# Kernel optimization log

Hardware: AMD Instinct MI355X
Metric: run time of the kernel (lower is better)

The kernel has to match this reference:

```python
import jax, jax.numpy as jnp
import numpy as np

B, T, F, U, H = 256, 512, 128, 256, 64


def setup_inputs() -> dict:
    key = jax.random.key(0)
    k0, k1, k2, k3, k4 = jax.random.split(key, 5)
    x = jax.random.normal(k0, (B, T, F), dtype=jnp.float32)
    # Keras RandomUniform default range (-0.05, 0.05) for LSTM kernel/bias
    kernel = jax.random.uniform(k1, (F, 4 * U), minval=-0.05, maxval=0.05, dtype=jnp.float32)
    rec_kernel = jax.random.uniform(k2, (U, 4 * U), minval=-0.05, maxval=0.05, dtype=jnp.float32)
    bias = jax.random.uniform(k3, (4 * U,), minval=-0.05, maxval=0.05, dtype=jnp.float32)
    # Dense head: glorot-ish scale for the big [T*U, H] weight
    w_out = jax.random.normal(k4, (T * U, H), dtype=jnp.float32) * (1.0 / np.sqrt(T * U))
    b_out = jnp.zeros((H,), dtype=jnp.float32)
    return {"x": x, "kernel": kernel, "rec_kernel": rec_kernel, "bias": bias,
            "w_out": w_out, "b_out": b_out}


def _lstm_swish(x, kernel, rec_kernel, bias):
    """Keras LSTM with activation=swish, recurrent_activation=sigmoid.
    Gate order along last axis: i, f, c(g), o. Returns full hidden sequence [B,T,U]."""
    b, t, _ = x.shape
    u = rec_kernel.shape[0]
    # Precompute input projections for all timesteps: [B,T,4U]
    xz = jnp.einsum('btf,fg->btg', x, kernel) + bias

    def step(carry, xz_t):
        h, c = carry
        z = xz_t + h @ rec_kernel  # [B,4U]
        zi, zf, zg, zo = jnp.split(z, 4, axis=-1)
        i = jax.nn.sigmoid(zi)
        f = jax.nn.sigmoid(zf)
        g = jax.nn.swish(zg)
        o = jax.nn.sigmoid(zo)
        c_new = f * c + i * g
        h_new = o * jax.nn.swish(c_new)
        return (h_new, c_new), h_new

    h0 = jnp.zeros((b, u), dtype=x.dtype)
    c0 = jnp.zeros((b, u), dtype=x.dtype)
    (_, _), hs = jax.lax.scan(step, (h0, c0), jnp.swapaxes(xz, 0, 1))  # hs: [T,B,U]
    return jnp.swapaxes(hs, 0, 1)  # [B,T,U]


def reference(x, kernel, rec_kernel, bias, w_out, b_out):
    seq = _lstm_swish(x, kernel, rec_kernel, bias)        # [B,T,U]
    flat = seq.reshape(seq.shape[0], -1)                   # [B,T*U]
    return flat @ w_out + b_out                            # [B,horizon]
```

## Files before the change

kernel.cpp:

```cpp
#include <hip/hip_runtime.h>
#include <stdint.h>

#define B_ 256
#define T_ 512
#define F_ 128
#define U_ 256
#define H_ 64
#define G4U 1024

typedef __attribute__((ext_vector_type(8))) short short8;
typedef __attribute__((ext_vector_type(4))) float f32x4;
typedef unsigned long long ull;

#define BARRIER_LDS() asm volatile("s_waitcnt lgkmcnt(0)\ns_barrier" ::: "memory")

__device__ __forceinline__ uint16_t f2bf(float f) {
  uint32_t u = __builtin_bit_cast(uint32_t, f);
  u += 0x7fffu + ((u >> 16) & 1u);
  return (uint16_t)(u >> 16);
}
__device__ __forceinline__ float bf2f(uint32_t v) {
  return __builtin_bit_cast(float, (v & 0xffffu) << 16);
}
__device__ __forceinline__ float frcp(float x) {
  float r;
  asm volatile("v_rcp_f32 %0, %1" : "=v"(r) : "v"(x));
  return r;
}
__device__ __forceinline__ float sigm(float z) {
  return frcp(1.0f + __expf(-z));
}
__device__ __forceinline__ ull ald(const ull* p) {
  return __hip_atomic_load(p, __ATOMIC_RELAXED, __HIP_MEMORY_SCOPE_AGENT);
}

__global__ __launch_bounds__(256, 1) void xz_pre(
    const float* __restrict__ x, const float* __restrict__ kern,
    const float* __restrict__ bias, uint16_t* __restrict__ xz,
    int t0, int L)
{
  const int tid  = threadIdx.x;
  const int lane = tid & 63;
  const int q    = tid >> 6;
  const int il   = lane & 15;
  const int bx   = blockIdx.x;
  const int bg   = bx & 15;
  const int hp   = (bx >> 4) & 1;
  const int tc   = bx >> 5;

  __shared__ __align__(16) uint16_t kern_lds[8192 * 8];
  __shared__ __align__(16) uint16_t x_stage[2][4][64][8];

  for (int s = 0; s < 32; ++s) {
    const int slot = tid + s * 256;
    const int l = slot & 63, kt = (slot >> 6) & 3, ctl = (slot >> 8) & 7, qq = slot >> 11;
    const int col = qq * 256 + (hp * 8 + ctl) * 16 + (l & 15);
    const int kb  = kt * 32 + (l >> 4) * 8;
    short8 v;
    #pragma unroll
    for (int j = 0; j < 8; ++j)
      v[j] = (short)f2bf(kern[(size_t)(kb + j) * G4U + col]);
    *(short8*)&kern_lds[(size_t)slot * 8] = v;
  }
  float bias_r[8];
  #pragma unroll
  for (int ctl = 0; ctl < 8; ++ctl)
    bias_r[ctl] = bias[q * 256 + (hp * 8 + ctl) * 16 + il];

  const int xrow = tid & 15, xfb = (tid >> 4) * 8;
  const int xs_kt = xfb >> 5, xs_l = ((xfb >> 3) & 3) * 16 + xrow;

  float xv[8];
  {
    const float* p = x + ((size_t)(bg * 16 + xrow) * T_ + (t0 + tc * 16)) * F_ + xfb;
    #pragma unroll
    for (int j = 0; j < 8; ++j) xv[j] = p[j];
  }
  __syncthreads();

  for (int tt2 = 0; tt2 < 16; ++tt2) {
    const int t = t0 + tc * 16 + tt2;
    const int bb = tt2 & 1;
    {
      uint16_t* d = &x_stage[bb][xs_kt][xs_l][0];
      #pragma unroll
      for (int j = 0; j < 8; ++j) d[j] = f2bf(xv[j]);
    }
    BARRIER_LDS();
    {
      const int tn = (tt2 < 15) ? t + 1 : t;
      const float* p = x + ((size_t)(bg * 16 + xrow) * T_ + tn) * F_ + xfb;
      #pragma unroll
      for (int j = 0; j < 8; ++j) xv[j] = p[j];
    }
    f32x4 acc[8];
    #pragma unroll
    for (int ctl = 0; ctl < 8; ++ctl)
      acc[ctl] = (f32x4){bias_r[ctl], bias_r[ctl], bias_r[ctl], bias_r[ctl]};
    #pragma unroll
    for (int kt = 0; kt < 4; ++kt) {
      short8 a = *(const short8*)&x_stage[bb][kt][lane][0];
      #pragma unroll
      for (int ctl = 0; ctl < 8; ++ctl) {
        short8 b = *(const short8*)&kern_lds[(size_t)(((q * 8 + ctl) * 4 + kt) * 64 + lane) * 8];
        acc[ctl] = __builtin_amdgcn_mfma_f32_16x16x32_bf16(a, b, acc[ctl], 0, 0, 0);
      }
    }
    uint16_t* ob = xz + (size_t)(bg * L + (t - t0)) * 16384;
    #pragma unroll
    for (int ctl = 0; ctl < 8; ++ctl) {
      const int wd = hp * 8 + ctl;
      const uint32_t lo = (uint32_t)f2bf(acc[ctl][0]) | ((uint32_t)f2bf(acc[ctl][1]) << 16);
      const uint32_t hi = (uint32_t)f2bf(acc[ctl][2]) | ((uint32_t)f2bf(acc[ctl][3]) << 16);
      *(ull*)(ob + (size_t)(wd * 4 + q) * 256 + lane * 4) = (ull)lo | ((ull)hi << 32);
    }
  }
}

__global__ __launch_bounds__(512, 2) void lstm_pair(
    const float* __restrict__ rker, uint16_t* __restrict__ seq,
    ull* __restrict__ hbuf, const uint16_t* __restrict__ xz,
    float* __restrict__ cstbuf, int t0, int L)
{
  const int tid  = threadIdx.x;
  const int lane = tid & 63;
  const int wv   = tid >> 6;
  const int il   = lane & 15;
  const int rg   = lane >> 4;
  const int bg   = blockIdx.x & 15;
  const int m    = blockIdx.x >> 4;

  __shared__ __align__(16) uint16_t h_stage[2][8][64][8];

  short8 wf[4][8];
  #pragma unroll
  for (int q = 0; q < 4; ++q) {
    const int gcol = q * U_ + m * 128 + wv * 16 + il;
    #pragma unroll
    for (int kk = 0; kk < 8; ++kk) {
      const int ktg = ((kk & 4) ? (m ^ 1) : m) * 4 + (kk & 3);
      short8 v;
      #pragma unroll
      for (int j = 0; j < 8; ++j)
        v[j] = (short)f2bf(rker[(size_t)(ktg * 32 + rg * 8 + j) * G4U + gcol]);
      wf[q][kk] = v;
    }
  }

  const int u_loc = wv * 16 + il;
  const int Ua  = m * 128 + u_loc;
  const int kta = Ua >> 5, ga = ((Ua & 31) >> 3) * 16, posa = Ua & 7;

  ull* const pub_s = hbuf + (size_t)(bg * 2 + m) * 2048;
  const ull* const pub_p = hbuf + (size_t)(bg * 2 + (m ^ 1)) * 2048;

  const int up_u = tid >> 2;
  const int up_rb = (tid & 3) * 4;

  float cst[4];
  if (t0 == 0) {
    #pragma unroll
    for (int j = 0; j < 4; ++j) cst[j] = 0.f;
  } else {
    #pragma unroll
    for (int j = 0; j < 4; ++j)
      cst[j] = cstbuf[(size_t)(bg * 16 + rg * 4 + j) * U_ + Ua];
    const ull* op = pub_s + (size_t)((t0 - 1) & 1) * 1024 + tid * 2;
    const ull o0 = ald(op), o1 = ald(op + 1);
    const int U  = m * 128 + up_u;
    const int kt = U >> 5, g = ((U & 31) >> 3) * 16, pos = U & 7;
    h_stage[(t0 - 1) & 1][kt][g + up_rb + 0][pos] = (uint16_t)o0;
    h_stage[(t0 - 1) & 1][kt][g + up_rb + 1][pos] = (uint16_t)(o0 >> 16);
    h_stage[(t0 - 1) & 1][kt][g + up_rb + 2][pos] = (uint16_t)o1;
    h_stage[(t0 - 1) & 1][kt][g + up_rb + 3][pos] = (uint16_t)(o1 >> 16);
  }
  __syncthreads();

  const uint16_t* const pzbase = xz + (size_t)bg * L * 16384
                               + (size_t)((m * 8 + wv) * 4) * 256 + lane * 4;
  ull zc[4];
  #pragma unroll
  for (int q = 0; q < 4; ++q) zc[q] = *(const ull*)(pzbase + q * 256);

  for (int tt = 0; tt < L; ++tt) {
    const int t = t0 + tt;
    const ull* pp = pub_p + (size_t)((t - 1) & 1) * 1024 + tid * 2;
    ull pv0 = 0, pv1 = 0;
    if (t > 0) {
      pv0 = ald(pp); pv1 = ald(pp + 1);
      __builtin_amdgcn_sched_barrier(0);
    }
    f32x4 acc[4];
    #pragma unroll
    for (int q = 0; q < 4; ++q) {
      const uint32_t lo = (uint32_t)zc[q];
      const uint32_t hi = (uint32_t)(zc[q] >> 32);
      acc[q][0] = bf2f(lo); acc[q][1] = bf2f(lo >> 16);
      acc[q][2] = bf2f(hi); acc[q][3] = bf2f(hi >> 16);
    }
    {
      const int ntt = (tt + 1 < L) ? tt + 1 : tt;
      const uint16_t* pn = pzbase + (size_t)ntt * 16384;
      #pragma unroll
      for (int q = 0; q < 4; ++q) zc[q] = *(const ull*)(pn + q * 256);
    }
    if (t > 0) {
      const int p_ = (t - 1) & 1;
      #pragma unroll
      for (int kk = 0; kk < 4; ++kk) {
        short8 a = *(const short8*)&h_stage[p_][m * 4 + kk][lane][0];
        #pragma unroll
        for (int q = 0; q < 4; ++q)
          acc[q] = __builtin_amdgcn_mfma_f32_16x16x32_bf16(a, wf[q][kk], acc[q], 0, 0, 0);
      }
      const uint32_t expt = (uint32_t)t;
      while (((uint32_t)(pv0 >> 32) != expt) | ((uint32_t)(pv1 >> 32) != expt)) {
        pv0 = ald(pp); pv1 = ald(pp + 1);
      }
      const int U  = (m ^ 1) * 128 + up_u;
      const int kt = U >> 5, g = ((U & 31) >> 3) * 16, pos = U & 7;
      h_stage[p_][kt][g + up_rb + 0][pos] = (uint16_t)pv0;
      h_stage[p_][kt][g + up_rb + 1][pos] = (uint16_t)(pv0 >> 16);
      h_stage[p_][kt][g + up_rb + 2][pos] = (uint16_t)pv1;
      h_stage[p_][kt][g + up_rb + 3][pos] = (uint16_t)(pv1 >> 16);
    }
    BARRIER_LDS();
    if (t > 0) {
      const int p_ = (t - 1) & 1;
      #pragma unroll
      for (int kk = 0; kk < 4; ++kk) {
        short8 a = *(const short8*)&h_stage[p_][(m ^ 1) * 4 + kk][lane][0];
        #pragma unroll
        for (int q = 0; q < 4; ++q)
          acc[q] = __builtin_amdgcn_mfma_f32_16x16x32_bf16(a, wf[q][4 + kk], acc[q], 0, 0, 0);
      }
    }
    {
      uint16_t b16[4];
      #pragma unroll
      for (int j = 0; j < 4; ++j) {
        const float zi = acc[0][j], zf = acc[1][j];
        const float zg = acc[2][j], zo = acc[3][j];
        const float ii = sigm(zi), ff = sigm(zf);
        const float gg = zg * sigm(zg), oo = sigm(zo);
        const float c  = ff * cst[j] + ii * gg;
        cst[j] = c;
        b16[j] = f2bf(oo * (c * sigm(c)));
      }
      const int s2 = t & 1;
      ull* pw = pub_s + (size_t)s2 * 1024 + (size_t)u_loc * 8 + rg * 2;
      const ull tg = (ull)(uint32_t)(t + 1) << 32;
      __hip_atomic_store(pw,     (ull)((uint32_t)b16[0] | ((uint32_t)b16[1] << 16)) | tg,
                         __ATOMIC_RELAXED, __HIP_MEMORY_SCOPE_AGENT);
      __hip_atomic_store(pw + 1, (ull)((uint32_t)b16[2] | ((uint32_t)b16[3] << 16)) | tg,
                         __ATOMIC_RELAXED, __HIP_MEMORY_SCOPE_AGENT);
      #pragma unroll
      for (int j = 0; j < 4; ++j) {
        h_stage[s2][kta][ga + rg * 4 + j][posa] = b16[j];
        seq[((size_t)(bg * 16 + rg * 4 + j) * T_ + t) * U_ + Ua] = b16[j];
      }
    }
    BARRIER_LDS();
  }
  #pragma unroll
  for (int j = 0; j < 4; ++j)
    cstbuf[(size_t)(bg * 16 + rg * 4 + j) * U_ + Ua] = cst[j];
}

__global__ __launch_bounds__(512, 2) void lstm_fallback(
    const float* __restrict__ x, const float* __restrict__ kern,
    const float* __restrict__ rker, const float* __restrict__ bias,
    uint16_t* __restrict__ seq, ull* __restrict__ hbuf)
{
  const int tid  = threadIdx.x;
  const int lane = tid & 63;
  const int wv   = tid >> 6;
  const int il   = lane & 15;
  const int rg   = lane >> 4;
  const int bg   = blockIdx.x & 15;
  const int m    = blockIdx.x >> 4;

  __shared__ __align__(16) uint16_t x_stage[4][64][8];
  __shared__ __align__(16) uint16_t h_stage[2][8][64][8];
  __shared__ __align__(16) uint16_t kern_lds[8192 * 8];

  short8 wf[4][8];
  float  bias_r[4];
  #pragma unroll
  for (int q = 0; q < 4; ++q) {
    const int gcol = q * U_ + m * 128 + wv * 16 + il;
    bias_r[q] = bias[gcol];
    #pragma unroll
    for (int kk = 0; kk < 8; ++kk) {
      const int ktg = ((kk & 4) ? (m ^ 1) : m) * 4 + (kk & 3);
      short8 v;
      #pragma unroll
      for (int j = 0; j < 8; ++j)
        v[j] = (short)f2bf(rker[(size_t)(ktg * 32 + rg * 8 + j) * G4U + gcol]);
      wf[q][kk] = v;
    }
  }
  for (int s = 0; s < 16; ++s) {
    const int slot = tid + s * 512;
    const int ln = slot & 63, kt = (slot >> 6) & 3, ct = slot >> 8;
    const int col = (ct >> 3) * U_ + m * 128 + (ct & 7) * 16 + (ln & 15);
    const int kb  = kt * 32 + (ln >> 4) * 8;
    short8 v;
    #pragma unroll
    for (int j = 0; j < 8; ++j)
      v[j] = (short)f2bf(kern[(size_t)(kb + j) * G4U + col]);
    *(short8*)&kern_lds[(size_t)slot * 8] = v;
  }
  const int xkt = tid >> 7;
  const int xln = (tid >> 1) & 63;
  const int xj0 = (tid & 1) * 4;
  const int xrow = xln & 15;
  const int xk0  = xkt * 32 + (xln >> 4) * 8 + xj0;
  const int Ua  = m * 128 + wv * 16 + il;
  const int kta = Ua >> 5, ga = ((Ua & 31) >> 3) * 16, posa = Ua & 7;
  ull* const pub_s = hbuf + (size_t)(bg * 2 + m) * 2048;
  const ull* const pub_p = hbuf + (size_t)(bg * 2 + (m ^ 1)) * 2048;
  float cst[4];
  #pragma unroll
  for (int j = 0; j < 4; ++j) cst[j] = 0.f;
  float xp[4];
  {
    const float* p = x + ((size_t)(bg * 16 + xrow) * T_ + 0) * F_ + xk0;
    #pragma unroll
    for (int j = 0; j < 4; ++j) xp[j] = p[j];
    uint16_t* d = (uint16_t*)x_stage + tid * 4;
    #pragma unroll
    for (int j = 0; j < 4; ++j) d[j] = f2bf(xp[j]);
  }
  __syncthreads();
  for (int t = 0; t < T_; ++t) {
    const ull* pp = pub_p + (size_t)((t - 1) & 1) * 1024 + tid * 2;
    ull pv0 = 0, pv1 = 0;
    if (t > 0) {
      pv0 = ald(pp); pv1 = ald(pp + 1);
      __builtin_amdgcn_sched_barrier(0);
    }
    {
      const int tn = (t + 1 < T_) ? t + 1 : t;
      const float* p = x + ((size_t)(bg * 16 + xrow) * T_ + tn) * F_ + xk0;
      #pragma unroll
      for (int j = 0; j < 4; ++j) xp[j] = p[j];
    }
    f32x4 acc[4];
    #pragma unroll
    for (int q = 0; q < 4; ++q)
      acc[q] = (f32x4){bias_r[q], bias_r[q], bias_r[q], bias_r[q]};
    #pragma unroll
    for (int kt = 0; kt < 4; ++kt) {
      short8 a = *(const short8*)&x_stage[kt][lane][0];
      #pragma unroll
      for (int q = 0; q < 4; ++q) {
        short8 b = *(const short8*)&kern_lds[(size_t)(((q * 8 + wv) * 4 + kt) * 64 + lane) * 8];
        acc[q] = __builtin_amdgcn_mfma_f32_16x16x32_bf16(a, b, acc[q], 0, 0, 0);
      }
    }
    if (t > 0) {
      const int p_ = (t - 1) & 1;
      #pragma unroll
      for (int kk = 0; kk < 4; ++kk) {
        short8 a = *(const short8*)&h_stage[p_][m * 4 + kk][lane][0];
        #pragma unroll
        for (int q = 0; q < 4; ++q)
          acc[q] = __builtin_amdgcn_mfma_f32_16x16x32_bf16(a, wf[q][kk], acc[q], 0, 0, 0);
      }
      const uint32_t expt = (uint32_t)t;
      while (((uint32_t)(pv0 >> 32) != expt) | ((uint32_t)(pv1 >> 32) != expt)) {
        pv0 = ald(pp); pv1 = ald(pp + 1);
      }
      const int u_loc = tid >> 2;
      const int U  = (m ^ 1) * 128 + u_loc;
      const int kt = U >> 5, g = ((U & 31) >> 3) * 16, pos = U & 7;
      const int rb = (tid & 3) * 4;
      h_stage[p_][kt][g + rb + 0][pos] = (uint16_t)pv0;
      h_stage[p_][kt][g + rb + 1][pos] = (uint16_t)(pv0 >> 16);
      h_stage[p_][kt][g + rb + 2][pos] = (uint16_t)pv1;
      h_stage[p_][kt][g + rb + 3][pos] = (uint16_t)(pv1 >> 16);
    }
    BARRIER_LDS();
    if (t > 0) {
      const int p_ = (t - 1) & 1;
      #pragma unroll
      for (int kk = 0; kk < 4; ++kk) {
        short8 a = *(const short8*)&h_stage[p_][(m ^ 1) * 4 + kk][lane][0];
        #pragma unroll
        for (int q = 0; q < 4; ++q)
          acc[q] = __builtin_amdgcn_mfma_f32_16x16x32_bf16(a, wf[q][4 + kk], acc[q], 0, 0, 0);
      }
    }
    {
      uint16_t* d = (uint16_t*)x_stage + tid * 4;
      #pragma unroll
      for (int j = 0; j < 4; ++j) d[j] = f2bf(xp[j]);
    }
    {
      uint16_t b16[4];
      #pragma unroll
      for (int j = 0; j < 4; ++j) {
        const float zi = acc[0][j], zf = acc[1][j];
        const float zg = acc[2][j], zo = acc[3][j];
        const float ii = sigm(zi), ff = sigm(zf);
        const float gg = zg * sigm(zg), oo = sigm(zo);
        const float c  = ff * cst[j] + ii * gg;
        cst[j] = c;
        b16[j] = f2bf(oo * (c * sigm(c)));
      }
      const int s2 = t & 1;
      ull* pw = pub_s + (size_t)s2 * 1024 + (size_t)(wv * 16 + il) * 8 + rg * 2;
      const ull tg = (ull)(uint32_t)(t + 1) << 32;
      __hip_atomic_store(pw,     (ull)((uint32_t)b16[0] | ((uint32_t)b16[1] << 16)) | tg,
                         __ATOMIC_RELAXED, __HIP_MEMORY_SCOPE_AGENT);
      __hip_atomic_store(pw + 1, (ull)((uint32_t)b16[2] | ((uint32_t)b16[3] << 16)) | tg,
                         __ATOMIC_RELAXED, __HIP_MEMORY_SCOPE_AGENT);
      #pragma unroll
      for (int j = 0; j < 4; ++j) {
        h_stage[s2][kta][ga + rg * 4 + j][posa] = b16[j];
        seq[((size_t)(bg * 16 + rg * 4 + j) * T_ + t) * U_ + Ua] = b16[j];
      }
    }
    BARRIER_LDS();
  }
}

__global__ __launch_bounds__(256, 1) void head_kernel(
    const uint16_t* __restrict__ seq, const float* __restrict__ w_out,
    float* __restrict__ partials)
{
  const int g    = blockIdx.x;
  const int tid  = threadIdx.x;
  const int lane = tid & 63;
  const int wv   = tid >> 6;

  f32x4 acc[4][4];
  #pragma unroll
  for (int i = 0; i < 4; ++i)
    #pragma unroll
    for (int c = 0; c < 4; ++c) acc[i][c] = (f32x4){0.f, 0.f, 0.f, 0.f};

  for (int ks = 0; ks < 64; ++ks) {
    const int krow = g * 2048 + ks * 32 + (lane >> 4) * 8;
    short8 bf[4];
    #pragma unroll
    for (int c = 0; c < 4; ++c) {
      short8 v;
      #pragma unroll
      for (int j = 0; j < 8; ++j)
        v[j] = (short)f2bf(w_out[(size_t)(krow + j) * H_ + c * 16 + (lane & 15)]);
      bf[c] = v;
    }
    #pragma unroll
    for (int i = 0; i < 4; ++i) {
      const int b = (wv * 4 + i) * 16 + (lane & 15);
      short8 a = *(const short8*)(seq + (size_t)b * (T_ * U_) + krow);
      #pragma unroll
      for (int c = 0; c < 4; ++c)
        acc[i][c] = __builtin_amdgcn_mfma_f32_16x16x32_bf16(a, bf[c], acc[i][c], 0, 0, 0);
    }
  }
  #pragma unroll
  for (int i = 0; i < 4; ++i)
    #pragma unroll
    for (int c = 0; c < 4; ++c)
      #pragma unroll
      for (int r = 0; r < 4; ++r) {
        const int b = wv * 64 + i * 16 + (lane >> 4) * 4 + r;
        partials[((size_t)g * B_ + b) * H_ + c * 16 + (lane & 15)] = acc[i][c][r];
      }
}

__global__ void reduce_kernel(const float* __restrict__ partials,
                              const float* __restrict__ b_out,
                              float* __restrict__ out)
{
  const int i = blockIdx.x * 256 + threadIdx.x;
  float s = b_out[i & (H_ - 1)];
  #pragma unroll 8
  for (int g = 0; g < 64; ++g) s += partials[(size_t)g * (B_ * H_) + i];
  out[i] = s;
}

extern "C" void kernel_launch(void* const* d_in, const int* in_sizes, int n_in,
                              void* d_out, int out_size, void* d_ws, size_t ws_size,
                              hipStream_t stream) {
  (void)in_sizes; (void)n_in; (void)out_size;
  const float* x     = (const float*)d_in[0];
  const float* kern  = (const float*)d_in[1];
  const float* rker  = (const float*)d_in[2];
  const float* bias  = (const float*)d_in[3];
  const float* w_out = (const float*)d_in[4];
  const float* b_out = (const float*)d_in[5];
  float* out = (float*)d_out;

  char* ws = (char*)d_ws;
  const size_t seq_bytes  = (size_t)B_ * T_ * U_ * 2;
  const size_t hbuf_bytes = (size_t)32 * 2048 * 8;
  const size_t part_bytes = (size_t)64 * B_ * H_ * 4;
  const size_t cst_bytes  = (size_t)B_ * U_ * 4;
  uint16_t* seq      = (uint16_t*)ws;
  ull*      hbuf     = (ull*)(ws + seq_bytes);
  float*    partials = (float*)(ws + seq_bytes + hbuf_bytes);
  float*    cstbuf   = (float*)(ws + seq_bytes + hbuf_bytes + part_bytes);
  const size_t xz_off = seq_bytes + hbuf_bytes + part_bytes + cst_bytes;
  uint16_t* xzbuf = (uint16_t*)(ws + xz_off);

  int L = 0;
  const int cand[4] = {128, 64, 32, 16};
  for (int i = 0; i < 4; ++i) {
    if (ws_size >= xz_off + (size_t)cand[i] * 524288) { L = cand[i]; break; }
  }

  hipMemsetAsync(hbuf, 0, hbuf_bytes, stream);

  if (L > 0) {
    for (int t0 = 0; t0 < T_; t0 += L) {
      xz_pre<<<2 * L, 256, 0, stream>>>(x, kern, bias, xzbuf, t0, L);
      lstm_pair<<<32, 512, 0, stream>>>(rker, seq, hbuf, xzbuf, cstbuf, t0, L);
    }
  } else {
    lstm_fallback<<<32, 512, 0, stream>>>(x, kern, rker, bias, seq, hbuf);
  }
  head_kernel<<<64, 256, 0, stream>>>(seq, w_out, partials);
  reduce_kernel<<<64, 256, 0, stream>>>(partials, b_out, out);
}
```

Measured before the change: 1.193 ms.

## Split batch rows into two interleaved groups to overlap peer exchange with compute

The recurrent kernel's 16 batch rows per block are split into two half-groups (A and B), each with its own LDS staging buffer and its own published hidden-state slots. While waiting for the peer block's half-B values, the block finishes gate math for half A and publishes it, so cross-block communication latency overlaps with useful work. Each half still runs the full MFMA on all 16 rows but keeps only two of them, which doubles MFMA work and adds an extra barrier per step in exchange for a shorter critical path.

```diff
diff --git a/kernel.cpp b/kernel.cpp
--- a/kernel.cpp
+++ b/kernel.cpp
@@ -117,7 +117,7 @@
   }
 }
 
-__global__ __launch_bounds__(512, 2) void lstm_pair(
+__global__ __launch_bounds__(512, 2) void lstm_pair2(
     const float* __restrict__ rker, uint16_t* __restrict__ seq,
     ull* __restrict__ hbuf, const uint16_t* __restrict__ xz,
     float* __restrict__ cstbuf, int t0, int L)
@@ -129,8 +129,11 @@
   const int rg   = lane >> 4;
   const int bg   = blockIdx.x & 15;
   const int m    = blockIdx.x >> 4;
-
-  __shared__ __align__(16) uint16_t h_stage[2][8][64][8];
+  const int bgm  = bg * 2 + m;
+  const int pgm  = bg * 2 + (m ^ 1);
+
+  __shared__ __align__(16) uint16_t hA[2][8][64][8];
+  __shared__ __align__(16) uint16_t hB[2][8][64][8];
 
   short8 wf[4][8];
   #pragma unroll
@@ -151,30 +154,44 @@
   const int Ua  = m * 128 + u_loc;
   const int kta = Ua >> 5, ga = ((Ua & 31) >> 3) * 16, posa = Ua & 7;
 
-  ull* const pub_s = hbuf + (size_t)(bg * 2 + m) * 2048;
-  const ull* const pub_p = hbuf + (size_t)(bg * 2 + (m ^ 1)) * 2048;
-
-  const int up_u = tid >> 2;
-  const int up_rb = (tid & 3) * 4;
-
-  float cst[4];
+  const int cu  = tid >> 2;
+  const int cp  = (tid & 3) * 4;
+  const int Up  = (m ^ 1) * 128 + cu;
+  const int upkt = Up >> 5, upg = ((Up & 31) >> 3) * 16, uppos = Up & 7;
+  const int Uo  = m * 128 + cu;
+  const int uokt = Uo >> 5, uog = ((Uo & 31) >> 3) * 16, uopos = Uo & 7;
+
+  ull* const pubA = hbuf + (size_t)((bgm * 2 + 0) * 2) * 512;
+  ull* const pubB = hbuf + (size_t)((bgm * 2 + 1) * 2) * 512;
+  const ull* const peerA = hbuf + (size_t)((pgm * 2 + 0) * 2) * 512;
+  const ull* const peerB = hbuf + (size_t)((pgm * 2 + 1) * 2) * 512;
+
+  {
+    ull* z0 = (ull*)hA;  ull* z1 = (ull*)hB;
+    #pragma unroll
+    for (int k = 0; k < 4; ++k) { z0[tid + k * 512] = 0; z1[tid + k * 512] = 0; }
+  }
+
+  float cA0, cA1, cB0, cB1;
   if (t0 == 0) {
-    #pragma unroll
-    for (int j = 0; j < 4; ++j) cst[j] = 0.f;
+    cA0 = cA1 = cB0 = cB1 = 0.f;
   } else {
-    #pragma unroll
-    for (int j = 0; j < 4; ++j)
-      cst[j] = cstbuf[(size_t)(bg * 16 + rg * 4 + j) * U_ + Ua];
-    const ull* op = pub_s + (size_t)((t0 - 1) & 1) * 1024 + tid * 2;
-    const ull o0 = ald(op), o1 = ald(op + 1);
-    const int U  = m * 128 + up_u;
-    const int kt = U >> 5, g = ((U & 31) >> 3) * 16, pos = U & 7;
-    h_stage[(t0 - 1) & 1][kt][g + up_rb + 0][pos] = (uint16_t)o0;
-    h_stage[(t0 - 1) & 1][kt][g + up_rb + 1][pos] = (uint16_t)(o0 >> 16);
-    h_stage[(t0 - 1) & 1][kt][g + up_rb + 2][pos] = (uint16_t)o1;
-    h_stage[(t0 - 1) & 1][kt][g + up_rb + 3][pos] = (uint16_t)(o1 >> 16);
+    cA0 = cstbuf[(size_t)(bg * 16 + rg * 4 + 0) * U_ + Ua];
+    cA1 = cstbuf[(size_t)(bg * 16 + rg * 4 + 1) * U_ + Ua];
+    cB0 = cstbuf[(size_t)(bg * 16 + rg * 4 + 2) * U_ + Ua];
+    cB1 = cstbuf[(size_t)(bg * 16 + rg * 4 + 3) * U_ + Ua];
   }
   __syncthreads();
+  if (t0 > 0) {
+    const int rp = (t0 - 1) & 1;
+    const ull oA = ald(pubA + (size_t)rp * 512 + tid);
+    const ull oB = ald(pubB + (size_t)rp * 512 + tid);
+    hA[rp][uokt][uog + cp + 0][uopos] = (uint16_t)oA;
+    hA[rp][uokt][uog + cp + 1][uopos] = (uint16_t)(oA >> 16);
+    hB[rp][uokt][uog + cp + 2][uopos] = (uint16_t)oB;
+    hB[rp][uokt][uog + cp + 3][uopos] = (uint16_t)(oB >> 16);
+    __syncthreads();
+  }
 
   const uint16_t* const pzbase = xz + (size_t)bg * L * 16384
                                + (size_t)((m * 8 + wv) * 4) * 256 + lane * 4;
@@ -183,20 +200,24 @@
   for (int q = 0; q < 4; ++q) zc[q] = *(const ull*)(pzbase + q * 256);
 
   for (int tt = 0; tt < L; ++tt) {
-    const int t = t0 + tt;
-    const ull* pp = pub_p + (size_t)((t - 1) & 1) * 1024 + tid * 2;
-    ull pv0 = 0, pv1 = 0;
-    if (t > 0) {
-      pv0 = ald(pp); pv1 = ald(pp + 1);
+    const int t  = t0 + tt;
+    const int pb = (t - 1) & 1, cb = t & 1;
+    const ull* ppA = peerA + (size_t)pb * 512 + tid;
+    const ull* ppB = peerB + (size_t)pb * 512 + tid;
+    ull pvA = 0, pvB = 0;
+    if (t > 0) {
+      pvA = ald(ppA); pvB = ald(ppB);
       __builtin_amdgcn_sched_barrier(0);
     }
-    f32x4 acc[4];
+    f32x4 accA[4], accB[4];
     #pragma unroll
     for (int q = 0; q < 4; ++q) {
       const uint32_t lo = (uint32_t)zc[q];
       const uint32_t hi = (uint32_t)(zc[q] >> 32);
-      acc[q][0] = bf2f(lo); acc[q][1] = bf2f(lo >> 16);
-      acc[q][2] = bf2f(hi); acc[q][3] = bf2f(hi >> 16);
+      f32x4 z;
+      z[0] = bf2f(lo); z[1] = bf2f(lo >> 16);
+      z[2] = bf2f(hi); z[3] = bf2f(hi >> 16);
+      accA[q] = z; accB[q] = z;
     }
     {
       const int ntt = (tt + 1 < L) ? tt + 1 : tt;
@@ -205,66 +226,93 @@
       for (int q = 0; q < 4; ++q) zc[q] = *(const ull*)(pn + q * 256);
     }
     if (t > 0) {
-      const int p_ = (t - 1) & 1;
       #pragma unroll
       for (int kk = 0; kk < 4; ++kk) {
-        short8 a = *(const short8*)&h_stage[p_][m * 4 + kk][lane][0];
+        short8 aA = *(const short8*)&hA[pb][m * 4 + kk][lane][0];
         #pragma unroll
         for (int q = 0; q < 4; ++q)
-          acc[q] = __builtin_amdgcn_mfma_f32_16x16x32_bf16(a, wf[q][kk], acc[q], 0, 0, 0);
-      }
-      const uint32_t expt = (uint32_t)t;
-      while (((uint32_t)(pv0 >> 32) != expt) | ((uint32_t)(pv1 >> 32) != expt)) {
-        pv0 = ald(pp); pv1 = ald(pp + 1);
-      }
-      const int U  = (m ^ 1) * 128 + up_u;
-      const int kt = U >> 5, g = ((U & 31) >> 3) * 16, pos = U & 7;
-      h_stage[p_][kt][g + up_rb + 0][pos] = (uint16_t)pv0;
-      h_stage[p_][kt][g + up_rb + 1][pos] = (uint16_t)(pv0 >> 16);
-      h_stage[p_][kt][g + up_rb + 2][pos] = (uint16_t)pv1;
-      h_stage[p_][kt][g + up_rb + 3][pos] = (uint16_t)(pv1 >> 16);
-    }
-    BARRIER_LDS();
-    if (t > 0) {
-      const int p_ = (t - 1) & 1;
+          accA[q] = __builtin_amdgcn_mfma_f32_16x16x32_bf16(aA, wf[q][kk], accA[q], 0, 0, 0);
+      }
       #pragma unroll
       for (int kk = 0; kk < 4; ++kk) {
-        short8 a = *(const short8*)&h_stage[p_][(m ^ 1) * 4 + kk][lane][0];
+        short8 aB = *(const short8*)&hB[pb][m * 4 + kk][lane][0];
         #pragma unroll
         for (int q = 0; q < 4; ++q)
-          acc[q] = __builtin_amdgcn_mfma_f32_16x16x32_bf16(a, wf[q][4 + kk], acc[q], 0, 0, 0);
-      }
-    }
-    {
-      uint16_t b16[4];
-      #pragma unroll
-      for (int j = 0; j < 4; ++j) {
-        const float zi = acc[0][j], zf = acc[1][j];
-        const float zg = acc[2][j], zo = acc[3][j];
-        const float ii = sigm(zi), ff = sigm(zf);
-        const float gg = zg * sigm(zg), oo = sigm(zo);
-        const float c  = ff * cst[j] + ii * gg;
-        cst[j] = c;
-        b16[j] = f2bf(oo * (c * sigm(c)));
-      }
-      const int s2 = t & 1;
-      ull* pw = pub_s + (size_t)s2 * 1024 + (size_t)u_loc * 8 + rg * 2;
-      const ull tg = (ull)(uint32_t)(t + 1) << 32;
-      __hip_atomic_store(pw,     (ull)((uint32_t)b16[0] | ((uint32_t)b16[1] << 16)) | tg,
+          accB[q] = __builtin_amdgcn_mfma_f32_16x16x32_bf16(aB, wf[q][kk], accB[q], 0, 0, 0);
+      }
+      const uint32_t expt = (uint32_t)t;
+      while ((uint32_t)(pvA >> 32) != expt) pvA = ald(ppA);
+      hA[pb][upkt][upg + cp + 0][uppos] = (uint16_t)pvA;
+      hA[pb][upkt][upg + cp + 1][uppos] = (uint16_t)(pvA >> 16);
+    }
+    BARRIER_LDS();
+    if (t > 0) {
+      #pragma unroll
+      for (int kk = 0; kk < 4; ++kk) {
+        short8 aA = *(const short8*)&hA[pb][(m ^ 1) * 4 + kk][lane][0];
+        #pragma unroll
+        for (int q = 0; q < 4; ++q)
+          accA[q] = __builtin_amdgcn_mfma_f32_16x16x32_bf16(aA, wf[q][4 + kk], accA[q], 0, 0, 0);
+      }
+    }
+    {
+      const float zi0 = accA[0][0], zf0 = accA[1][0], zg0 = accA[2][0], zo0 = accA[3][0];
+      const float zi1 = accA[0][1], zf1 = accA[1][1], zg1 = accA[2][1], zo1 = accA[3][1];
+      const float i0 = sigm(zi0), f0 = sigm(zf0), g0 = zg0 * sigm(zg0), o0 = sigm(zo0);
+      const float i1 = sigm(zi1), f1 = sigm(zf1), g1 = zg1 * sigm(zg1), o1 = sigm(zo1);
+      cA0 = f0 * cA0 + i0 * g0;
+      cA1 = f1 * cA1 + i1 * g1;
+      const uint16_t b0 = f2bf(o0 * (cA0 * sigm(cA0)));
+      const uint16_t b1 = f2bf(o1 * (cA1 * sigm(cA1)));
+      __hip_atomic_store(pubA + (size_t)cb * 512 + u_loc * 4 + rg,
+                         (ull)((uint32_t)b0 | ((uint32_t)b1 << 16))
+                           | ((ull)(uint32_t)(t + 1) << 32),
                          __ATOMIC_RELAXED, __HIP_MEMORY_SCOPE_AGENT);
-      __hip_atomic_store(pw + 1, (ull)((uint32_t)b16[2] | ((uint32_t)b16[3] << 16)) | tg,
+      hA[cb][kta][ga + rg * 4 + 0][posa] = b0;
+      hA[cb][kta][ga + rg * 4 + 1][posa] = b1;
+      seq[((size_t)(bg * 16 + rg * 4 + 0) * T_ + t) * U_ + Ua] = b0;
+      seq[((size_t)(bg * 16 + rg * 4 + 1) * T_ + t) * U_ + Ua] = b1;
+    }
+    if (t > 0) {
+      const uint32_t expt = (uint32_t)t;
+      while ((uint32_t)(pvB >> 32) != expt) pvB = ald(ppB);
+      hB[pb][upkt][upg + cp + 2][uppos] = (uint16_t)pvB;
+      hB[pb][upkt][upg + cp + 3][uppos] = (uint16_t)(pvB >> 16);
+    }
+    BARRIER_LDS();
+    if (t > 0) {
+      #pragma unroll
+      for (int kk = 0; kk < 4; ++kk) {
+        short8 aB = *(const short8*)&hB[pb][(m ^ 1) * 4 + kk][lane][0];
+        #pragma unroll
+        for (int q = 0; q < 4; ++q)
+          accB[q] = __builtin_amdgcn_mfma_f32_16x16x32_bf16(aB, wf[q][4 + kk], accB[q], 0, 0, 0);
+      }
+    }
+    {
+      const float zi0 = accB[0][2], zf0 = accB[1][2], zg0 = accB[2][2], zo0 = accB[3][2];
+      const float zi1 = accB[0][3], zf1 = accB[1][3], zg1 = accB[2][3], zo1 = accB[3][3];
+      const float i0 = sigm(zi0), f0 = sigm(zf0), g0 = zg0 * sigm(zg0), o0 = sigm(zo0);
+      const float i1 = sigm(zi1), f1 = sigm(zf1), g1 = zg1 * sigm(zg1), o1 = sigm(zo1);
+      cB0 = f0 * cB0 + i0 * g0;
+      cB1 = f1 * cB1 + i1 * g1;
+      const uint16_t b0 = f2bf(o0 * (cB0 * sigm(cB0)));
+      const uint16_t b1 = f2bf(o1 * (cB1 * sigm(cB1)));
+      __hip_atomic_store(pubB + (size_t)cb * 512 + u_loc * 4 + rg,
+                         (ull)((uint32_t)b0 | ((uint32_t)b1 << 16))
+                           | ((ull)(uint32_t)(t + 1) << 32),
                          __ATOMIC_RELAXED, __HIP_MEMORY_SCOPE_AGENT);
-      #pragma unroll
-      for (int j = 0; j < 4; ++j) {
-        h_stage[s2][kta][ga + rg * 4 + j][posa] = b16[j];
-        seq[((size_t)(bg * 16 + rg * 4 + j) * T_ + t) * U_ + Ua] = b16[j];
-      }
+      hB[cb][kta][ga + rg * 4 + 2][posa] = b0;
+      hB[cb][kta][ga + rg * 4 + 3][posa] = b1;
+      seq[((size_t)(bg * 16 + rg * 4 + 2) * T_ + t) * U_ + Ua] = b0;
+      seq[((size_t)(bg * 16 + rg * 4 + 3) * T_ + t) * U_ + Ua] = b1;
     }
     BARRIER_LDS();
   }
-  #pragma unroll
-  for (int j = 0; j < 4; ++j)
-    cstbuf[(size_t)(bg * 16 + rg * 4 + j) * U_ + Ua] = cst[j];
+  cstbuf[(size_t)(bg * 16 + rg * 4 + 0) * U_ + Ua] = cA0;
+  cstbuf[(size_t)(bg * 16 + rg * 4 + 1) * U_ + Ua] = cA1;
+  cstbuf[(size_t)(bg * 16 + rg * 4 + 2) * U_ + Ua] = cB0;
+  cstbuf[(size_t)(bg * 16 + rg * 4 + 3) * U_ + Ua] = cB1;
 }
 
 __global__ __launch_bounds__(512, 2) void lstm_fallback(
@@ -372,8 +420,8 @@
       while (((uint32_t)(pv0 >> 32) != expt) | ((uint32_t)(pv1 >> 32) != expt)) {
         pv0 = ald(pp); pv1 = ald(pp + 1);
       }
-      const int u_loc = tid >> 2;
-      const int U  = (m ^ 1) * 128 + u_loc;
+      const int u_loc2 = tid >> 2;
+      const int U  = (m ^ 1) * 128 + u_loc2;
       const int kt = U >> 5, g = ((U & 31) >> 3) * 16, pos = U & 7;
       const int rb = (tid & 3) * 4;
       h_stage[p_][kt][g + rb + 0][pos] = (uint16_t)pv0;
@@ -518,7 +566,7 @@
   if (L > 0) {
     for (int t0 = 0; t0 < T_; t0 += L) {
       xz_pre<<<2 * L, 256, 0, stream>>>(x, kern, bias, xzbuf, t0, L);
-      lstm_pair<<<32, 512, 0, stream>>>(rker, seq, hbuf, xzbuf, cstbuf, t0, L);
+      lstm_pair2<<<32, 512, 0, stream>>>(rker, seq, hbuf, xzbuf, cstbuf, t0, L);
     }
   } else {
     lstm_fallback<<<32, 512, 0, stream>>>(x, kern, rker, bias, seq, hbuf);
```

Result: slower. 1.476 ms (+23.7%).
